# Kernel tuning notes

Hardware: AMD Instinct MI355X
Metric: run time of the kernel (lower is better)

The kernel has to match this reference:

```python
import jax, jax.numpy as jnp
import numpy as np

N_NODES = 50000

def _sage_mean(x, src, tgt, Wl, bl, Wr):
    # PyG SAGEConv(aggr='mean'): out = lin_l(mean_{j in N(i)} x_j) + lin_r(x_i)
    # aggregate in input dim first (cheaper), then transform
    agg = jax.ops.segment_sum(x[src], tgt, num_segments=N_NODES)  # [N, Din]
    deg = jax.ops.segment_sum(jnp.ones((src.shape[0],), x.dtype), tgt, num_segments=N_NODES)
    mean = agg / jnp.maximum(deg, 1.0)[:, None]
    return mean @ Wl + bl + x @ Wr

def setup_inputs() -> dict:
    key = jax.random.key(0)
    ks = jax.random.split(key, 16)
    d_in, d0, d1 = 64, 256, 128  # input, initial_channels=2*128, hidden
    d_out = 8
    s = 0.02
    x = jax.random.normal(ks[0], (N_NODES, d_in), dtype=jnp.float32)
    edge_index = jax.random.randint(ks[1], (2, 800000), 0, N_NODES, dtype=jnp.int64)
    p = lambda k, sh: s * jax.random.normal(k, sh, dtype=jnp.float32)
    return {
        "x": x, "edge_index": edge_index,
        # first_conv: 64 -> 256
        "Wf_l": p(ks[2], (d_in, d0)), "bf": jnp.zeros((d0,), jnp.float32), "Wf_r": p(ks[3], (d_in, d0)),
        # conv0: 256 -> 128
        "W0_l": p(ks[4], (d0, d1)), "b0": jnp.zeros((d1,), jnp.float32), "W0_r": p(ks[5], (d0, d1)),
        # conv1: 128 -> 128
        "W1_l": p(ks[6], (d1, d1)), "b1": jnp.zeros((d1,), jnp.float32), "W1_r": p(ks[7], (d1, d1)),
        # head MLP
        "W_lin": p(ks[8], (d1, d1)), "b_lin": jnp.zeros((d1,), jnp.float32),
        "W_lin2": p(ks[9], (d1, d_out)), "b_lin2": jnp.zeros((d_out,), jnp.float32),
    }

def reference(x, edge_index, Wf_l, bf, Wf_r, W0_l, b0, W0_r, W1_l, b1, W1_r, W_lin, b_lin, W_lin2, b_lin2):
    src, tgt = edge_index[0], edge_index[1]
    h = jax.nn.relu(_sage_mean(x, src, tgt, Wf_l, bf, Wf_r))
    h = jax.nn.relu(_sage_mean(h, src, tgt, W0_l, b0, W0_r))
    h = jax.nn.relu(_sage_mean(h, src, tgt, W1_l, b1, W1_r))
    h = h @ W_lin + b_lin
    return h @ W_lin2 + b_lin2
```

## Files before the change

kernel.cpp:

```cpp
#include <hip/hip_runtime.h>
#include <hip/hip_fp16.h>


typedef __attribute__((ext_vector_type(8))) short bf16x8;
typedef __attribute__((ext_vector_type(4))) float f32x4;

struct Seg { const unsigned short* A; const unsigned short* W; int lda; int ldw; int K; };
struct Segs { Seg s[4]; int n; };

__device__ __forceinline__ unsigned short f2bf(float x) {
  unsigned u = __float_as_uint(x);
  u += 0x7FFF + ((u >> 16) & 1);
  return (unsigned short)(u >> 16);
}
__device__ __forceinline__ unsigned short f2h(float x) {
  return __half_as_ushort(__float2half(x));
}
__device__ __forceinline__ float2 ld_h2(const unsigned short* p, size_t idx) {
  unsigned uv = *(const unsigned*)(p + idx);
  __half2 h = *reinterpret_cast<__half2*>(&uv);
  return __half22float2(h);
}


__global__ __launch_bounds__(256) void hist_k(const int* __restrict__ tgt, int* __restrict__ histT,
                                              int E, int NB, int CH) {
  extern __shared__ int sh[];
  int g = blockIdx.x, tid = threadIdx.x;
  for (int b = tid; b < NB; b += 256) sh[b] = 0;
  __syncthreads();
  int eb = g * CH, ee = min(eb + CH, E);
  for (int i = eb + tid; i < ee; i += 256)
    atomicAdd(&sh[tgt[i] >> 6], 1);
  __syncthreads();
  for (int b = tid; b < NB; b += 256) histT[b * 64 + g] = sh[b];
}

__global__ __launch_bounds__(256) void scanb_k(int* __restrict__ histT, int* __restrict__ bcnt, int NB) {
  int wv = threadIdx.x >> 6, lane = threadIdx.x & 63;
  int b = blockIdx.x * 4 + wv;
  if (b >= NB) return;
  int v = histT[b * 64 + lane];
  int x = v;
#pragma unroll
  for (int o = 1; o < 64; o <<= 1) {
    int y = __shfl_up(x, o);
    if (lane >= o) x += y;
  }
  histT[b * 64 + lane] = x - v;
  if (lane == 63) bcnt[b] = x;
}

__global__ __launch_bounds__(1024) void bscan_k(const int* __restrict__ bcnt, int* __restrict__ boff,
                                                int* __restrict__ row_ptr, int NB, int E, int N) {
  __shared__ int sh[1024];
  int tid = threadIdx.x;
  int v = (tid < NB) ? bcnt[tid] : 0;
  int val = v;
  sh[tid] = val;
  __syncthreads();
  for (int o = 1; o < 1024; o <<= 1) {
    int t = (tid >= o) ? sh[tid - o] : 0;
    __syncthreads();
    val += t;
    sh[tid] = val;
    __syncthreads();
  }
  if (tid < NB) boff[tid] = val - v;
  if (tid == NB - 1) boff[NB] = val;
  if (tid == 0) row_ptr[N] = E;
}

__global__ __launch_bounds__(256) void scatter_k(const int* __restrict__ src, const int* __restrict__ tgt,
                                                 const int* __restrict__ boff, const int* __restrict__ histT,
                                                 unsigned* __restrict__ vals, int E, int NB, int CH) {
  extern __shared__ int sh[];
  int g = blockIdx.x, tid = threadIdx.x;
  for (int b = tid; b < NB; b += 256) sh[b] = boff[b] + histT[b * 64 + g];
  __syncthreads();
  int eb = g * CH, ee = min(eb + CH, E);
  for (int i = eb + tid; i < ee; i += 256) {
    int t = tgt[i], s = src[i];
    int pos = atomicAdd(&sh[t >> 6], 1);
    vals[pos] = (unsigned)s | ((unsigned)(t & 63) << 17);
  }
}

__global__ __launch_bounds__(256) void bsort_k(const unsigned* __restrict__ vals, const int* __restrict__ boff,
                                               int* __restrict__ row_ptr, int* __restrict__ srcs, int N) {
  int b = blockIdx.x;
  int base = b << 6;
  int s0 = boff[b], s1 = boff[b + 1];
  __shared__ int hist[64], excl[64], cur[64];
  int tid = threadIdx.x;
  if (tid < 64) { hist[tid] = 0; cur[tid] = 0; }
  __syncthreads();
  for (int i = s0 + tid; i < s1; i += 256)
    atomicAdd(&hist[(vals[i] >> 17) & 63], 1);
  __syncthreads();
  if (tid < 64) {
    int v = hist[tid];
    int x = v;
#pragma unroll
    for (int o = 1; o < 64; o <<= 1) {
      int y = __shfl_up(x, o);
      if (tid >= o) x += y;
    }
    excl[tid] = x - v;
    int node = base + tid;
    if (node < N) row_ptr[node] = s0 + x - v;
  }
  __syncthreads();
  for (int i = s0 + tid; i < s1; i += 256) {
    unsigned v = vals[i];
    int l = (v >> 17) & 63;
    int pos = s0 + excl[l] + atomicAdd(&cur[l], 1);
    srcs[pos] = (int)(v & 0x1FFFF);
  }
}

__device__ __forceinline__ void split_store(float v, unsigned short* hi, unsigned short* lo, int idx) {
  unsigned short h = f2bf(v);
  float hf = __uint_as_float(((unsigned)h) << 16);
  hi[idx] = h;
  lo[idx] = f2bf(v - hf);
}

__global__ __launch_bounds__(256) void prep_k(
    const float* __restrict__ x, unsigned short* __restrict__ xb, unsigned short* __restrict__ xh, int nbConv, int n4,
    const float* __restrict__ Wf_l, const float* __restrict__ Wf_r,
    unsigned short* __restrict__ Wt1hi, unsigned short* __restrict__ Wt1lo,
    const float* __restrict__ W0_l, const float* __restrict__ W0_r, unsigned short* __restrict__ Wt2hi,
    const float* __restrict__ W1_l, const float* __restrict__ W1_r, unsigned short* __restrict__ Wt3hi,
    const float* __restrict__ Wlin, const float* __restrict__ blin,
    const float* __restrict__ Wlin2, const float* __restrict__ blin2,
    float* __restrict__ Wc, float* __restrict__ bc) {
  int b = blockIdx.x, t = threadIdx.x;
  if (b < nbConv) {
    int i = b * 256 + t;
    if (i < n4) {
      float4 v = ((const float4*)x)[i];
      ((ushort2*)xb)[i * 2]     = make_ushort2(f2bf(v.x), f2bf(v.y));
      ((ushort2*)xb)[i * 2 + 1] = make_ushort2(f2bf(v.z), f2bf(v.w));
      ((ushort2*)xh)[i * 2]     = make_ushort2(f2h(v.x), f2h(v.y));
      ((ushort2*)xh)[i * 2 + 1] = make_ushort2(f2h(v.z), f2h(v.w));
    }
    return;
  }
  b -= nbConv;
  if (b < 128) {
    int idx = b * 256 + t;
    int n = idx >> 7, k = idx & 127;
    float v = (k < 64) ? Wf_l[k * 256 + n] : Wf_r[(k - 64) * 256 + n];
    split_store(v, Wt1hi, Wt1lo, idx);
    return;
  }
  b -= 128;
  if (b < 256) {
    int idx = b * 256 + t;
    int n = idx >> 8, k = idx & 255;
    float v = (n < 128) ? W0_l[k * 128 + n] : W0_r[k * 128 + (n - 128)];
    Wt2hi[idx] = f2bf(v);
    return;
  }
  b -= 256;
  if (b < 128) {
    int idx = b * 256 + t;
    int n = idx >> 7, k = idx & 127;
    float v = (n < 128) ? W1_l[k * 128 + n] : W1_r[k * 128 + (n - 128)];
    Wt3hi[idx] = f2bf(v);
    return;
  }
  b -= 128;
  {
    int idx = b * 256 + t;
    if (idx < 1024) {
      int i = idx >> 3, j = idx & 7;
      float acc = 0.f;
      for (int k = 0; k < 128; ++k) acc = fmaf(Wlin[i * 128 + k], Wlin2[k * 8 + j], acc);
      Wc[idx] = acc;
    }
    if (idx < 8) {
      float acc = blin2[idx];
      for (int k = 0; k < 128; ++k) acc = fmaf(blin[k], Wlin2[k * 8 + idx], acc);
      bc[idx] = acc;
    }
  }
}

__global__ __launch_bounds__(256) void agg_mean64_k(const unsigned short* __restrict__ xh, const int* __restrict__ rp,
                                                    const int* __restrict__ srcs, unsigned short* __restrict__ mb, int n) {
  int w = threadIdx.x >> 6, lane = threadIdx.x & 63;
  int node = blockIdx.x * 4 + w;
  if (node >= n) return;
  int s0 = rp[node], s1 = rp[node + 1];
  float sum = 0.f;
  int e = s0;
  for (; e + 7 < s1; e += 8) {
    int i0 = srcs[e], i1 = srcs[e + 1], i2 = srcs[e + 2], i3 = srcs[e + 3];
    int i4 = srcs[e + 4], i5 = srcs[e + 5], i6 = srcs[e + 6], i7 = srcs[e + 7];
    float v0 = __half2float(__ushort_as_half(xh[(size_t)i0 * 64 + lane]));
    float v1 = __half2float(__ushort_as_half(xh[(size_t)i1 * 64 + lane]));
    float v2 = __half2float(__ushort_as_half(xh[(size_t)i2 * 64 + lane]));
    float v3 = __half2float(__ushort_as_half(xh[(size_t)i3 * 64 + lane]));
    float v4 = __half2float(__ushort_as_half(xh[(size_t)i4 * 64 + lane]));
    float v5 = __half2float(__ushort_as_half(xh[(size_t)i5 * 64 + lane]));
    float v6 = __half2float(__ushort_as_half(xh[(size_t)i6 * 64 + lane]));
    float v7 = __half2float(__ushort_as_half(xh[(size_t)i7 * 64 + lane]));
    sum += ((v0 + v1) + (v2 + v3)) + ((v4 + v5) + (v6 + v7));
  }
  for (; e < s1; ++e)
    sum += __half2float(__ushort_as_half(xh[(size_t)srcs[e] * 64 + lane]));
  int deg = s1 - s0;
  float inv = 1.f / (float)(deg > 0 ? deg : 1);
  mb[(size_t)node * 64 + lane] = f2bf(sum * inv);
}

template <int OUTMODE>
__global__ __launch_bounds__(256) void agg128_k(const unsigned short* __restrict__ yb,
                                                const unsigned short* __restrict__ zb,
                                                const float* __restrict__ bias,
                                                const int* __restrict__ rp, const int* __restrict__ srcs,
                                                void* __restrict__ hout,
                                                const float* __restrict__ Wc, const float* __restrict__ bc, int n) {
  int w = threadIdx.x >> 6, lane = threadIdx.x & 63;
  int node = blockIdx.x * 4 + w;
  if (node >= n) return;
  int s0 = rp[node], s1 = rp[node + 1];
  int d = lane * 2;
  float sx = 0.f, sy = 0.f;
  int e = s0;
  for (; e + 7 < s1; e += 8) {
    int i0 = srcs[e], i1 = srcs[e + 1], i2 = srcs[e + 2], i3 = srcs[e + 3];
    int i4 = srcs[e + 4], i5 = srcs[e + 5], i6 = srcs[e + 6], i7 = srcs[e + 7];
    float2 v0 = ld_h2(yb, (size_t)i0 * 128 + d);
    float2 v1 = ld_h2(yb, (size_t)i1 * 128 + d);
    float2 v2 = ld_h2(yb, (size_t)i2 * 128 + d);
    float2 v3 = ld_h2(yb, (size_t)i3 * 128 + d);
    float2 v4 = ld_h2(yb, (size_t)i4 * 128 + d);
    float2 v5 = ld_h2(yb, (size_t)i5 * 128 + d);
    float2 v6 = ld_h2(yb, (size_t)i6 * 128 + d);
    float2 v7 = ld_h2(yb, (size_t)i7 * 128 + d);
    sx += ((v0.x + v1.x) + (v2.x + v3.x)) + ((v4.x + v5.x) + (v6.x + v7.x));
    sy += ((v0.y + v1.y) + (v2.y + v3.y)) + ((v4.y + v5.y) + (v6.y + v7.y));
  }
  for (; e < s1; ++e) {
    float2 v = ld_h2(yb, (size_t)srcs[e] * 128 + d);
    sx += v.x; sy += v.y;
  }
  int deg = s1 - s0;
  float inv = 1.f / (float)(deg > 0 ? deg : 1);
  float2 z = ld_h2(zb, (size_t)node * 128 + d);
  float2 b2 = *(const float2*)&bias[d];
  float ox = fmaxf(fmaf(sx, inv, z.x + b2.x), 0.f);
  float oy = fmaxf(fmaf(sy, inv, z.y + b2.y), 0.f);

  if (OUTMODE == 1) {
    ((ushort2*)hout)[((size_t)node * 128 + d) / 2] = make_ushort2(f2bf(ox), f2bf(oy));
  } else {
    const float4* wr = (const float4*)&Wc[d * 8];
    float4 wa0 = wr[0], wa1 = wr[1], wb0 = wr[2], wb1 = wr[3];
    float a8[8];
    a8[0] = ox * wa0.x + oy * wb0.x;
    a8[1] = ox * wa0.y + oy * wb0.y;
    a8[2] = ox * wa0.z + oy * wb0.z;
    a8[3] = ox * wa0.w + oy * wb0.w;
    a8[4] = ox * wa1.x + oy * wb1.x;
    a8[5] = ox * wa1.y + oy * wb1.y;
    a8[6] = ox * wa1.z + oy * wb1.z;
    a8[7] = ox * wa1.w + oy * wb1.w;
#pragma unroll
    for (int off = 32; off >= 1; off >>= 1) {
#pragma unroll
      for (int j = 0; j < 8; ++j) a8[j] += __shfl_xor(a8[j], off);
    }
    if (lane == 0) {
      float* o = (float*)hout + (size_t)node * 8;
      *(float4*)o       = make_float4(a8[0] + bc[0], a8[1] + bc[1], a8[2] + bc[2], a8[3] + bc[3]);
      *(float4*)(o + 4) = make_float4(a8[4] + bc[4], a8[5] + bc[5], a8[6] + bc[6], a8[7] + bc[7]);
    }
  }
}

template <int MODE>
__global__ __launch_bounds__(256) void gemm_mfma_k(Segs segs, const float* __restrict__ bias,
                                                   unsigned short* __restrict__ Y, unsigned short* __restrict__ Z,
                                                   unsigned short* __restrict__ Ob, int ldc) {
  __shared__ unsigned short Asl[128 * 32];
  __shared__ unsigned short Wsl[128 * 32];
  int tid = threadIdx.x;
  int lane = tid & 63, wave = tid >> 6;
  int wm = wave & 1, wn = wave >> 1;
  int rowBase = blockIdx.x * 128, colBase = blockIdx.y * 128;
  f32x4 acc[4][4] = {};

  int c0 = tid, c1 = tid + 256;
  int r0 = c0 >> 2, q0 = c0 & 3;
  int r1 = c1 >> 2, q1 = c1 & 3;
  int ml = lane & 15, qq = lane >> 4;

  for (int si = 0; si < segs.n; ++si) {
    const unsigned short* Aseg = segs.s[si].A;
    const unsigned short* Wseg = segs.s[si].W;
    int lda = segs.s[si].lda, ldw = segs.s[si].ldw, K = segs.s[si].K;
    for (int k0 = 0; k0 < K; k0 += 32) {
      uint4 av0 = *(const uint4*)&Aseg[(size_t)(rowBase + r0) * lda + k0 + q0 * 8];
      uint4 av1 = *(const uint4*)&Aseg[(size_t)(rowBase + r1) * lda + k0 + q1 * 8];
      uint4 wv0 = *(const uint4*)&Wseg[(size_t)(colBase + r0) * ldw + k0 + q0 * 8];
      uint4 wv1 = *(const uint4*)&Wseg[(size_t)(colBase + r1) * ldw + k0 + q1 * 8];
      __syncthreads();
      *(uint4*)&Asl[c0 * 8] = av0;
      *(uint4*)&Asl[c1 * 8] = av1;
      *(uint4*)&Wsl[c0 * 8] = wv0;
      *(uint4*)&Wsl[c1 * 8] = wv1;
      __syncthreads();
      bf16x8 af[4], bw[4];
#pragma unroll
      for (int i = 0; i < 4; ++i) {
        af[i] = *(bf16x8*)&Asl[(wm * 64 + i * 16 + ml) * 32 + qq * 8];
        bw[i] = *(bf16x8*)&Wsl[(wn * 64 + i * 16 + ml) * 32 + qq * 8];
      }
#pragma unroll
      for (int mf = 0; mf < 4; ++mf)
#pragma unroll
        for (int nf = 0; nf < 4; ++nf)
          acc[mf][nf] = __builtin_amdgcn_mfma_f32_16x16x32_bf16(af[mf], bw[nf], acc[mf][nf], 0, 0, 0);
    }
  }

  if (MODE == 0) {
    unsigned short* dst = (colBase == 0) ? Y : Z;
#pragma unroll
    for (int mf = 0; mf < 4; ++mf) {
      int row = rowBase + wm * 64 + mf * 16 + qq * 4;
#pragma unroll
      for (int nf = 0; nf < 4; ++nf) {
        int col = wn * 64 + nf * 16 + ml;
#pragma unroll
        for (int r = 0; r < 4; ++r)
          dst[(size_t)(row + r) * 128 + col] = f2h(acc[mf][nf][r]);
      }
    }
  } else {
    float bc4[4];
#pragma unroll
    for (int nf = 0; nf < 4; ++nf) bc4[nf] = bias[colBase + wn * 64 + nf * 16 + ml];
#pragma unroll
    for (int mf = 0; mf < 4; ++mf) {
      int row = rowBase + wm * 64 + mf * 16 + qq * 4;
#pragma unroll
      for (int nf = 0; nf < 4; ++nf) {
        int col = colBase + wn * 64 + nf * 16 + ml;
#pragma unroll
        for (int r = 0; r < 4; ++r) {
          float o = fmaxf(acc[mf][nf][r] + bc4[nf], 0.f);
          Ob[(size_t)(row + r) * ldc + col] = f2bf(o);
        }
      }
    }
  }
}

extern "C" void kernel_launch(void* const* d_in, const int* in_sizes, int n_in,
                              void* d_out, int out_size, void* d_ws, size_t ws_size,
                              hipStream_t stream) {
  const float* x      = (const float*)d_in[0];
  const int*   ei     = (const int*)d_in[1];
  const float* Wf_l   = (const float*)d_in[2];
  const float* bf     = (const float*)d_in[3];
  const float* Wf_r   = (const float*)d_in[4];
  const float* W0_l   = (const float*)d_in[5];
  const float* b0     = (const float*)d_in[6];
  const float* W0_r   = (const float*)d_in[7];
  const float* W1_l   = (const float*)d_in[8];
  const float* b1     = (const float*)d_in[9];
  const float* W1_r   = (const float*)d_in[10];
  const float* W_lin  = (const float*)d_in[11];
  const float* b_lin  = (const float*)d_in[12];
  const float* W_lin2 = (const float*)d_in[13];
  const float* b_lin2 = (const float*)d_in[14];
  float* out = (float*)d_out;

  const int N = in_sizes[0] / 64;
  const int E = in_sizes[1] / 2;
  const int Npad = ((N + 127) / 128) * 128;
  const int nblkM = Npad / 128;
  const int NB = (N + 63) / 64;
  const int G  = 64;
  const int CH = (E + G - 1) / G;
  const int* e_src = ei;
  const int* e_tgt = ei + E;

  size_t off = 0;
  char* base = (char*)d_ws;
  auto carve = [&](size_t bytes) -> void* {
    void* p = base + off;
    off += (bytes + 255) & ~(size_t)255;
    return p;
  };
  int*      row_ptr = (int*)carve((size_t)(N + 1) * 4);
  int*      bcnt    = (int*)carve((size_t)NB * 4);
  int*      boff    = (int*)carve((size_t)(NB + 1) * 4);
  int*      histT   = (int*)carve((size_t)NB * G * 4);
  unsigned* vals    = (unsigned*)carve((size_t)E * 4);
  int*      srcs    = (int*)carve((size_t)E * 4);
  unsigned short* xb    = (unsigned short*)carve((size_t)Npad * 64 * 2);
  unsigned short* xh    = (unsigned short*)carve((size_t)Npad * 64 * 2);
  unsigned short* mb    = (unsigned short*)carve((size_t)Npad * 64 * 2);
  unsigned short* h1b   = (unsigned short*)carve((size_t)Npad * 256 * 2);
  unsigned short* h2b   = (unsigned short*)carve((size_t)Npad * 128 * 2);
  unsigned short* yb    = (unsigned short*)carve((size_t)Npad * 128 * 2);
  unsigned short* zb    = (unsigned short*)carve((size_t)Npad * 128 * 2);
  unsigned short* Wt1hi = (unsigned short*)carve(256 * 128 * 2);
  unsigned short* Wt1lo = (unsigned short*)carve(256 * 128 * 2);
  unsigned short* Wt2hi = (unsigned short*)carve(256 * 256 * 2);
  unsigned short* Wt3hi = (unsigned short*)carve(256 * 128 * 2);
  float* Wcomb = (float*)carve(1024 * 4);
  float* bcomb = (float*)carve(8 * 4);
  (void)ws_size; (void)n_in; (void)out_size;

  const int nbConv = (N * 16 + 255) / 256;
  const size_t ldsNB = (size_t)NB * 4;

  hist_k<<<G, 256, ldsNB, stream>>>(e_tgt, histT, E, NB, CH);
  scanb_k<<<(NB + 3) / 4, 256, 0, stream>>>(histT, bcnt, NB);
  bscan_k<<<1, 1024, 0, stream>>>(bcnt, boff, row_ptr, NB, E, N);
  scatter_k<<<G, 256, ldsNB, stream>>>(e_src, e_tgt, boff, histT, vals, E, NB, CH);
  bsort_k<<<NB, 256, 0, stream>>>(vals, boff, row_ptr, srcs, N);

  prep_k<<<nbConv + 128 + 256 + 128 + 4, 256, 0, stream>>>(
      x, xb, xh, nbConv, N * 16,
      Wf_l, Wf_r, Wt1hi, Wt1lo,
      W0_l, W0_r, Wt2hi,
      W1_l, W1_r, Wt3hi,
      W_lin, b_lin, W_lin2, b_lin2, Wcomb, bcomb);

  const int nbAgg = (N + 3) / 4;
  const dim3 gemmGrid(nblkM, 2);

  agg_mean64_k<<<nbAgg, 256, 0, stream>>>(xh, row_ptr, srcs, mb, N);
  {
    Segs s;
    s.n = 4;
    s.s[0] = {mb, Wt1hi,      64, 128, 64};
    s.s[1] = {xb, Wt1hi + 64, 64, 128, 64};
    s.s[2] = {mb, Wt1lo,      64, 128, 64};
    s.s[3] = {xb, Wt1lo + 64, 64, 128, 64};
    gemm_mfma_k<1><<<gemmGrid, 256, 0, stream>>>(s, bf, nullptr, nullptr, h1b, 256);
  }

  {
    Segs s;
    s.n = 1;
    s.s[0] = {h1b, Wt2hi, 256, 256, 256};
    s.s[1] = {nullptr, nullptr, 0, 0, 0};
    s.s[2] = {nullptr, nullptr, 0, 0, 0};
    s.s[3] = {nullptr, nullptr, 0, 0, 0};
    gemm_mfma_k<0><<<gemmGrid, 256, 0, stream>>>(s, nullptr, yb, zb, nullptr, 256);
  }
  agg128_k<1><<<nbAgg, 256, 0, stream>>>(yb, zb, b0, row_ptr, srcs, h2b, nullptr, nullptr, N);

  {
    Segs s;
    s.n = 1;
    s.s[0] = {h2b, Wt3hi, 128, 128, 128};
    s.s[1] = {nullptr, nullptr, 0, 0, 0};
    s.s[2] = {nullptr, nullptr, 0, 0, 0};
    s.s[3] = {nullptr, nullptr, 0, 0, 0};
    gemm_mfma_k<0><<<gemmGrid, 256, 0, stream>>>(s, nullptr, yb, zb, nullptr, 256);
  }
  agg128_k<2><<<nbAgg, 256, 0, stream>>>(yb, zb, b1, row_ptr, srcs, out, Wcomb, bcomb, N);
}
```

Before: 315.6 us.

## Fuse bucket sort into prep kernel, drop hi/lo weight split, widen gather unroll

Merges the per-bucket sort kernel and the prep kernel into one launch, saving a launch and letting the two independent jobs overlap. Drops the bf16 hi/lo split for the first-layer weights, which halves the first GEMM's segments at some cost in accuracy. The first aggregation now gathers fp32 x directly instead of a separate fp16 copy. Both gather loops unroll to 16 edges, with a masked, index-clamped tail in place of the scalar remainder loop, to keep more loads in flight. The fp32 gather reads twice the bytes per row, and the unroll adds register pressure.

```diff
diff --git a/kernel.cpp b/kernel.cpp
--- a/kernel.cpp
+++ b/kernel.cpp
@@ -21,7 +21,6 @@
   __half2 h = *reinterpret_cast<__half2*>(&uv);
   return __half22float2(h);
 }
-
 
 __global__ __launch_bounds__(256) void hist_k(const int* __restrict__ tgt, int* __restrict__ histT,
                                               int E, int NB, int CH) {
@@ -86,78 +85,68 @@
   }
 }
 
-__global__ __launch_bounds__(256) void bsort_k(const unsigned* __restrict__ vals, const int* __restrict__ boff,
-                                               int* __restrict__ row_ptr, int* __restrict__ srcs, int N) {
-  int b = blockIdx.x;
-  int base = b << 6;
-  int s0 = boff[b], s1 = boff[b + 1];
-  __shared__ int hist[64], excl[64], cur[64];
-  int tid = threadIdx.x;
-  if (tid < 64) { hist[tid] = 0; cur[tid] = 0; }
-  __syncthreads();
-  for (int i = s0 + tid; i < s1; i += 256)
-    atomicAdd(&hist[(vals[i] >> 17) & 63], 1);
-  __syncthreads();
-  if (tid < 64) {
-    int v = hist[tid];
-    int x = v;
-#pragma unroll
-    for (int o = 1; o < 64; o <<= 1) {
-      int y = __shfl_up(x, o);
-      if (tid >= o) x += y;
-    }
-    excl[tid] = x - v;
-    int node = base + tid;
-    if (node < N) row_ptr[node] = s0 + x - v;
-  }
-  __syncthreads();
-  for (int i = s0 + tid; i < s1; i += 256) {
-    unsigned v = vals[i];
-    int l = (v >> 17) & 63;
-    int pos = s0 + excl[l] + atomicAdd(&cur[l], 1);
-    srcs[pos] = (int)(v & 0x1FFFF);
-  }
-}
-
-__device__ __forceinline__ void split_store(float v, unsigned short* hi, unsigned short* lo, int idx) {
-  unsigned short h = f2bf(v);
-  float hf = __uint_as_float(((unsigned)h) << 16);
-  hi[idx] = h;
-  lo[idx] = f2bf(v - hf);
-}
-
-__global__ __launch_bounds__(256) void prep_k(
-    const float* __restrict__ x, unsigned short* __restrict__ xb, unsigned short* __restrict__ xh, int nbConv, int n4,
-    const float* __restrict__ Wf_l, const float* __restrict__ Wf_r,
-    unsigned short* __restrict__ Wt1hi, unsigned short* __restrict__ Wt1lo,
+__global__ __launch_bounds__(256) void bsort_prep_k(
+    const unsigned* __restrict__ vals, const int* __restrict__ boff,
+    int* __restrict__ row_ptr, int* __restrict__ srcs, int N, int NB,
+    const float* __restrict__ x, unsigned short* __restrict__ xb, int nbConv, int n4,
+    const float* __restrict__ Wf_l, const float* __restrict__ Wf_r, unsigned short* __restrict__ Wt1hi,
     const float* __restrict__ W0_l, const float* __restrict__ W0_r, unsigned short* __restrict__ Wt2hi,
     const float* __restrict__ W1_l, const float* __restrict__ W1_r, unsigned short* __restrict__ Wt3hi,
     const float* __restrict__ Wlin, const float* __restrict__ blin,
     const float* __restrict__ Wlin2, const float* __restrict__ blin2,
     float* __restrict__ Wc, float* __restrict__ bc) {
-  int b = blockIdx.x, t = threadIdx.x;
+  int b = blockIdx.x, tid = threadIdx.x;
+  if (b < NB) {
+    int base = b << 6;
+    int s0 = boff[b], s1 = boff[b + 1];
+    __shared__ int hist[64], excl[64], cur[64];
+    if (tid < 64) { hist[tid] = 0; cur[tid] = 0; }
+    __syncthreads();
+    for (int i = s0 + tid; i < s1; i += 256)
+      atomicAdd(&hist[(vals[i] >> 17) & 63], 1);
+    __syncthreads();
+    if (tid < 64) {
+      int v = hist[tid];
+      int xx = v;
+#pragma unroll
+      for (int o = 1; o < 64; o <<= 1) {
+        int y = __shfl_up(xx, o);
+        if (tid >= o) xx += y;
+      }
+      excl[tid] = xx - v;
+      int node = base + tid;
+      if (node < N) row_ptr[node] = s0 + xx - v;
+    }
+    __syncthreads();
+    for (int i = s0 + tid; i < s1; i += 256) {
+      unsigned v = vals[i];
+      int l = (v >> 17) & 63;
+      int pos = s0 + excl[l] + atomicAdd(&cur[l], 1);
+      srcs[pos] = (int)(v & 0x1FFFF);
+    }
+    return;
+  }
+  b -= NB;
   if (b < nbConv) {
-    int i = b * 256 + t;
+    int i = b * 256 + tid;
     if (i < n4) {
       float4 v = ((const float4*)x)[i];
       ((ushort2*)xb)[i * 2]     = make_ushort2(f2bf(v.x), f2bf(v.y));
       ((ushort2*)xb)[i * 2 + 1] = make_ushort2(f2bf(v.z), f2bf(v.w));
-      ((ushort2*)xh)[i * 2]     = make_ushort2(f2h(v.x), f2h(v.y));
-      ((ushort2*)xh)[i * 2 + 1] = make_ushort2(f2h(v.z), f2h(v.w));
     }
     return;
   }
   b -= nbConv;
   if (b < 128) {
-    int idx = b * 256 + t;
+    int idx = b * 256 + tid;
     int n = idx >> 7, k = idx & 127;
     float v = (k < 64) ? Wf_l[k * 256 + n] : Wf_r[(k - 64) * 256 + n];
-    split_store(v, Wt1hi, Wt1lo, idx);
+    Wt1hi[idx] = f2bf(v);
     return;
   }
   b -= 128;
   if (b < 256) {
-    int idx = b * 256 + t;
+    int idx = b * 256 + tid;
     int n = idx >> 8, k = idx & 255;
     float v = (n < 128) ? W0_l[k * 128 + n] : W0_r[k * 128 + (n - 128)];
     Wt2hi[idx] = f2bf(v);
@@ -165,7 +154,7 @@
   }
   b -= 256;
   if (b < 128) {
-    int idx = b * 256 + t;
+    int idx = b * 256 + tid;
     int n = idx >> 7, k = idx & 127;
     float v = (n < 128) ? W1_l[k * 128 + n] : W1_r[k * 128 + (n - 128)];
     Wt3hi[idx] = f2bf(v);
@@ -173,7 +162,7 @@
   }
   b -= 128;
   {
-    int idx = b * 256 + t;
+    int idx = b * 256 + tid;
     if (idx < 1024) {
       int i = idx >> 3, j = idx & 7;
       float acc = 0.f;
@@ -188,7 +177,7 @@
   }
 }
 
-__global__ __launch_bounds__(256) void agg_mean64_k(const unsigned short* __restrict__ xh, const int* __restrict__ rp,
+__global__ __launch_bounds__(256) void agg_mean64_k(const float* __restrict__ x, const int* __restrict__ rp,
                                                     const int* __restrict__ srcs, unsigned short* __restrict__ mb, int n) {
   int w = threadIdx.x >> 6, lane = threadIdx.x & 63;
   int node = blockIdx.x * 4 + w;
@@ -196,21 +185,34 @@
   int s0 = rp[node], s1 = rp[node + 1];
   float sum = 0.f;
   int e = s0;
-  for (; e + 7 < s1; e += 8) {
-    int i0 = srcs[e], i1 = srcs[e + 1], i2 = srcs[e + 2], i3 = srcs[e + 3];
-    int i4 = srcs[e + 4], i5 = srcs[e + 5], i6 = srcs[e + 6], i7 = srcs[e + 7];
-    float v0 = __half2float(__ushort_as_half(xh[(size_t)i0 * 64 + lane]));
-    float v1 = __half2float(__ushort_as_half(xh[(size_t)i1 * 64 + lane]));
-    float v2 = __half2float(__ushort_as_half(xh[(size_t)i2 * 64 + lane]));
-    float v3 = __half2float(__ushort_as_half(xh[(size_t)i3 * 64 + lane]));
-    float v4 = __half2float(__ushort_as_half(xh[(size_t)i4 * 64 + lane]));
-    float v5 = __half2float(__ushort_as_half(xh[(size_t)i5 * 64 + lane]));
-    float v6 = __half2float(__ushort_as_half(xh[(size_t)i6 * 64 + lane]));
-    float v7 = __half2float(__ushort_as_half(xh[(size_t)i7 * 64 + lane]));
-    sum += ((v0 + v1) + (v2 + v3)) + ((v4 + v5) + (v6 + v7));
-  }
-  for (; e < s1; ++e)
-    sum += __half2float(__ushort_as_half(xh[(size_t)srcs[e] * 64 + lane]));
+  for (; e + 16 <= s1; e += 16) {
+    int idx[16];
+#pragma unroll
+    for (int i = 0; i < 16; ++i) idx[i] = srcs[e + i];
+    float v[16];
+#pragma unroll
+    for (int i = 0; i < 16; ++i) v[i] = x[(size_t)idx[i] * 64 + lane];
+    float t0 = ((v[0] + v[1]) + (v[2] + v[3])) + ((v[4] + v[5]) + (v[6] + v[7]));
+    float t1 = ((v[8] + v[9]) + (v[10] + v[11])) + ((v[12] + v[13]) + (v[14] + v[15]));
+    sum += t0 + t1;
+  }
+  int rem = s1 - e;
+  if (rem > 0) {
+    int last = s1 - 1;
+    int idx[16];
+    idx[0] = srcs[e];
+#pragma unroll
+    for (int i = 1; i < 16; ++i) idx[i] = srcs[min(e + i, last)];
+    float v[16];
+#pragma unroll
+    for (int i = 0; i < 16; ++i) v[i] = x[(size_t)idx[i] * 64 + lane];
+    sum += v[0];
+#pragma unroll
+    for (int i = 1; i < 16; ++i) {
+      float m = (rem > i) ? 1.f : 0.f;
+      sum = fmaf(m, v[i], sum);
+    }
+  }
   int deg = s1 - s0;
   float inv = 1.f / (float)(deg > 0 ? deg : 1);
   mb[(size_t)node * 64 + lane] = f2bf(sum * inv);
@@ -230,23 +232,37 @@
   int d = lane * 2;
   float sx = 0.f, sy = 0.f;
   int e = s0;
-  for (; e + 7 < s1; e += 8) {
-    int i0 = srcs[e], i1 = srcs[e + 1], i2 = srcs[e + 2], i3 = srcs[e + 3];
-    int i4 = srcs[e + 4], i5 = srcs[e + 5], i6 = srcs[e + 6], i7 = srcs[e + 7];
-    float2 v0 = ld_h2(yb, (size_t)i0 * 128 + d);
-    float2 v1 = ld_h2(yb, (size_t)i1 * 128 + d);
-    float2 v2 = ld_h2(yb, (size_t)i2 * 128 + d);
-    float2 v3 = ld_h2(yb, (size_t)i3 * 128 + d);
-    float2 v4 = ld_h2(yb, (size_t)i4 * 128 + d);
-    float2 v5 = ld_h2(yb, (size_t)i5 * 128 + d);
-    float2 v6 = ld_h2(yb, (size_t)i6 * 128 + d);
-    float2 v7 = ld_h2(yb, (size_t)i7 * 128 + d);
-    sx += ((v0.x + v1.x) + (v2.x + v3.x)) + ((v4.x + v5.x) + (v6.x + v7.x));
-    sy += ((v0.y + v1.y) + (v2.y + v3.y)) + ((v4.y + v5.y) + (v6.y + v7.y));
-  }
-  for (; e < s1; ++e) {
-    float2 v = ld_h2(yb, (size_t)srcs[e] * 128 + d);
-    sx += v.x; sy += v.y;
+  for (; e + 16 <= s1; e += 16) {
+    int idx[16];
+#pragma unroll
+    for (int i = 0; i < 16; ++i) idx[i] = srcs[e + i];
+    float2 v[16];
+#pragma unroll
+    for (int i = 0; i < 16; ++i) v[i] = ld_h2(yb, (size_t)idx[i] * 128 + d);
+    float tx0 = ((v[0].x + v[1].x) + (v[2].x + v[3].x)) + ((v[4].x + v[5].x) + (v[6].x + v[7].x));
+    float tx1 = ((v[8].x + v[9].x) + (v[10].x + v[11].x)) + ((v[12].x + v[13].x) + (v[14].x + v[15].x));
+    float ty0 = ((v[0].y + v[1].y) + (v[2].y + v[3].y)) + ((v[4].y + v[5].y) + (v[6].y + v[7].y));
+    float ty1 = ((v[8].y + v[9].y) + (v[10].y + v[11].y)) + ((v[12].y + v[13].y) + (v[14].y + v[15].y));
+    sx += tx0 + tx1;
+    sy += ty0 + ty1;
+  }
+  int rem = s1 - e;
+  if (rem > 0) {
+    int last = s1 - 1;
+    int idx[16];
+    idx[0] = srcs[e];
+#pragma unroll
+    for (int i = 1; i < 16; ++i) idx[i] = srcs[min(e + i, last)];
+    float2 v[16];
+#pragma unroll
+    for (int i = 0; i < 16; ++i) v[i] = ld_h2(yb, (size_t)idx[i] * 128 + d);
+    sx += v[0].x; sy += v[0].y;
+#pragma unroll
+    for (int i = 1; i < 16; ++i) {
+      float m = (rem > i) ? 1.f : 0.f;
+      sx = fmaf(m, v[i].x, sx);
+      sy = fmaf(m, v[i].y, sy);
+    }
   }
   int deg = s1 - s0;
   float inv = 1.f / (float)(deg > 0 ? deg : 1);
@@ -405,14 +421,12 @@
   unsigned* vals    = (unsigned*)carve((size_t)E * 4);
   int*      srcs    = (int*)carve((size_t)E * 4);
   unsigned short* xb    = (unsigned short*)carve((size_t)Npad * 64 * 2);
-  unsigned short* xh    = (unsigned short*)carve((size_t)Npad * 64 * 2);
   unsigned short* mb    = (unsigned short*)carve((size_t)Npad * 64 * 2);
   unsigned short* h1b   = (unsigned short*)carve((size_t)Npad * 256 * 2);
   unsigned short* h2b   = (unsigned short*)carve((size_t)Npad * 128 * 2);
   unsigned short* yb    = (unsigned short*)carve((size_t)Npad * 128 * 2);
   unsigned short* zb    = (unsigned short*)carve((size_t)Npad * 128 * 2);
   unsigned short* Wt1hi = (unsigned short*)carve(256 * 128 * 2);
-  unsigned short* Wt1lo = (unsigned short*)carve(256 * 128 * 2);
   unsigned short* Wt2hi = (unsigned short*)carve(256 * 256 * 2);
   unsigned short* Wt3hi = (unsigned short*)carve(256 * 128 * 2);
   float* Wcomb = (float*)carve(1024 * 4);
@@ -420,17 +434,17 @@
   (void)ws_size; (void)n_in; (void)out_size;
 
   const int nbConv = (N * 16 + 255) / 256;
+  const int nbPrep = nbConv + 128 + 256 + 128 + 4;
   const size_t ldsNB = (size_t)NB * 4;
 
   hist_k<<<G, 256, ldsNB, stream>>>(e_tgt, histT, E, NB, CH);
   scanb_k<<<(NB + 3) / 4, 256, 0, stream>>>(histT, bcnt, NB);
   bscan_k<<<1, 1024, 0, stream>>>(bcnt, boff, row_ptr, NB, E, N);
   scatter_k<<<G, 256, ldsNB, stream>>>(e_src, e_tgt, boff, histT, vals, E, NB, CH);
-  bsort_k<<<NB, 256, 0, stream>>>(vals, boff, row_ptr, srcs, N);
-
-  prep_k<<<nbConv + 128 + 256 + 128 + 4, 256, 0, stream>>>(
-      x, xb, xh, nbConv, N * 16,
-      Wf_l, Wf_r, Wt1hi, Wt1lo,
+  bsort_prep_k<<<NB + nbPrep, 256, 0, stream>>>(
+      vals, boff, row_ptr, srcs, N, NB,
+      x, xb, nbConv, N * 16,
+      Wf_l, Wf_r, Wt1hi,
       W0_l, W0_r, Wt2hi,
       W1_l, W1_r, Wt3hi,
       W_lin, b_lin, W_lin2, b_lin2, Wcomb, bcomb);
@@ -438,14 +452,14 @@
   const int nbAgg = (N + 3) / 4;
   const dim3 gemmGrid(nblkM, 2);
 
-  agg_mean64_k<<<nbAgg, 256, 0, stream>>>(xh, row_ptr, srcs, mb, N);
+  agg_mean64_k<<<nbAgg, 256, 0, stream>>>(x, row_ptr, srcs, mb, N);
   {
     Segs s;
-    s.n = 4;
+    s.n = 2;
     s.s[0] = {mb, Wt1hi,      64, 128, 64};
     s.s[1] = {xb, Wt1hi + 64, 64, 128, 64};
-    s.s[2] = {mb, Wt1lo,      64, 128, 64};
-    s.s[3] = {xb, Wt1lo + 64, 64, 128, 64};
+    s.s[2] = {nullptr, nullptr, 0, 0, 0};
+    s.s[3] = {nullptr, nullptr, 0, 0, 0};
     gemm_mfma_k<1><<<gemmGrid, 256, 0, stream>>>(s, bf, nullptr, nullptr, h1b, 256);
   }
 
```

Result: faster. 283.6 us (-10.1%).
